# Optimization experiments

Measured on AMD Instinct MI355X. Metric: run time of the kernel, lower is better.

## Reference

```python
import jax, jax.numpy as jnp
import numpy as np

B, S, E, L = 4, 4096, 1024, 64
SCALE = float(np.sqrt(L))


def setup_inputs() -> dict:
    key = jax.random.key(0)
    ks = jax.random.split(key, 7)
    x = jax.random.normal(ks[0], (B, S, E), dtype=jnp.float32)
    # causal mask: positions with mask==0 are disallowed (masked_fill semantics)
    mask = jnp.tril(jnp.ones((S, S), dtype=jnp.int32))
    # Linear params (torch Linear: y = x @ W.T + b); store as [E, L] for x @ W
    sd = 1.0 / np.sqrt(E)
    Wq = jax.random.uniform(ks[1], (E, L), jnp.float32, -sd, sd)
    Wk = jax.random.uniform(ks[2], (E, L), jnp.float32, -sd, sd)
    Wv = jax.random.uniform(ks[3], (E, L), jnp.float32, -sd, sd)
    bq = jax.random.uniform(ks[4], (L,), jnp.float32, -sd, sd)
    bk = jax.random.uniform(ks[5], (L,), jnp.float32, -sd, sd)
    bv = jax.random.uniform(ks[6], (L,), jnp.float32, -sd, sd)
    return {"x": x, "Wq": Wq, "Wk": Wk, "Wv": Wv,
            "bq": bq, "bk": bk, "bv": bv, "mask": mask}


def reference(x, Wq, Wk, Wv, bq, bk, bv, mask):
    # Q,K,V: [B, S, L]
    Q = x @ Wq + bq
    K = x @ Wk + bk
    V = x @ Wv + bv
    # scores: [B, S, S] -- naive full matrix, faithful to the original
    scores = jnp.einsum('bsl,btl->bst', Q, K) / SCALE
    scores = jnp.where(mask == 0, -jnp.inf, scores)
    attn = jax.nn.softmax(scores, axis=-1)
    return jnp.einsum('bst,btl->bsl', attn, V)
```

## Files before the change

kernel.cpp:

```cpp
#include <hip/hip_runtime.h>
#include <hip/hip_bf16.h>
#include <cstdint>

typedef __bf16 bf16_t;
typedef __bf16 bf16x8 __attribute__((ext_vector_type(8)));
typedef float f32x4 __attribute__((ext_vector_type(4)));

#define B_ 4
#define S_ 4096
#define E_ 1024
#define L_ 64

__device__ __forceinline__ f32x4 mfma16(bf16x8 a, bf16x8 b, f32x4 c) {
  return __builtin_amdgcn_mfma_f32_16x16x32_bf16(a, b, c, 0, 0, 0);
}

template <int CTRL>
__device__ __forceinline__ float dpp_max_step(float x) {
  int t = __builtin_amdgcn_update_dpp(0, __float_as_int(x), CTRL, 0xF, 0xF, true);
  return fmaxf(x, __int_as_float(t));
}
template <int CTRL>
__device__ __forceinline__ float dpp_add_step(float x) {
  int t = __builtin_amdgcn_update_dpp(0, __float_as_int(x), CTRL, 0xF, 0xF, true);
  return x + __int_as_float(t);
}
__device__ __forceinline__ float dpp_reduce_max16(float x) {
  x = dpp_max_step<0x121>(x);
  x = dpp_max_step<0x122>(x);
  x = dpp_max_step<0x124>(x);
  x = dpp_max_step<0x128>(x);
  return x;
}
__device__ __forceinline__ float dpp_reduce_add16(float x) {
  x = dpp_add_step<0x121>(x);
  x = dpp_add_step<0x122>(x);
  x = dpp_add_step<0x124>(x);
  x = dpp_add_step<0x128>(x);
  return x;
}


__global__ void prep_w_kernel(const float* __restrict__ Wq, const float* __restrict__ Wk,
                              const float* __restrict__ Wv, bf16_t* __restrict__ Wf) {
  int n = blockIdx.x;
  const float* W = (n < 64) ? Wq : (n < 128 ? Wk : Wv);
  int col = n & 63;
  int nt = n >> 4, lr = n & 15;
  for (int k = threadIdx.x; k < E_; k += blockDim.x) {
    int kt = k >> 5, lg = (k >> 3) & 3, e = k & 7;
    Wf[((size_t)((nt * 32 + kt) * 64 + lg * 16 + lr) << 3) + e] = (bf16_t)W[(size_t)k * L_ + col];
  }
}

__global__ __launch_bounds__(512) void qkv_proj_kernel(
    const float* __restrict__ x, const bf16_t* __restrict__ Wf,
    const float* __restrict__ bq, const float* __restrict__ bk, const float* __restrict__ bv,
    bf16_t* __restrict__ Qf, bf16_t* __restrict__ Kf, bf16_t* __restrict__ Vf) {
  __shared__ float xs[2][32][68];

  const int tid = threadIdx.x;
  const int w = tid >> 6, l = tid & 63;
  const int lr = l & 15, lg = l >> 4;
  const int rowgrp = w & 1, colgrp = w >> 1;
  const int m0b = blockIdx.x * 32;
  const int srow = tid >> 4, scol = (tid & 15) * 4;

  f32x4 acc[3];
#pragma unroll
  for (int t = 0; t < 3; ++t) acc[t] = f32x4{0.f, 0.f, 0.f, 0.f};

  const float* xsrc = x + (size_t)(m0b + srow) * E_ + scol;
  {
    float4 r = *reinterpret_cast<const float4*>(xsrc);
    *reinterpret_cast<float4*>(&xs[0][srow][scol]) = r;
  }
  __syncthreads();

  int buf = 0;
  for (int kc = 0; kc < E_; kc += 64) {
    float4 nx;
    const bool have = (kc + 64) < E_;
    if (have) nx = *reinterpret_cast<const float4*>(xsrc + kc + 64);

    const float* xr = &xs[buf][rowgrp * 16 + lr][0];
    float4 f0 = *reinterpret_cast<const float4*>(xr + lg * 8);
    float4 f1 = *reinterpret_cast<const float4*>(xr + lg * 8 + 4);
    float4 f2 = *reinterpret_cast<const float4*>(xr + 32 + lg * 8);
    float4 f3 = *reinterpret_cast<const float4*>(xr + 32 + lg * 8 + 4);
    bf16x8 a0, a1;
    a0[0] = (bf16_t)f0.x; a0[1] = (bf16_t)f0.y; a0[2] = (bf16_t)f0.z; a0[3] = (bf16_t)f0.w;
    a0[4] = (bf16_t)f1.x; a0[5] = (bf16_t)f1.y; a0[6] = (bf16_t)f1.z; a0[7] = (bf16_t)f1.w;
    a1[0] = (bf16_t)f2.x; a1[1] = (bf16_t)f2.y; a1[2] = (bf16_t)f2.z; a1[3] = (bf16_t)f2.w;
    a1[4] = (bf16_t)f3.x; a1[5] = (bf16_t)f3.y; a1[6] = (bf16_t)f3.z; a1[7] = (bf16_t)f3.w;

    const int kt0 = kc >> 5;
#pragma unroll
    for (int t = 0; t < 3; ++t) {
      const int nt = colgrp * 3 + t;
      bf16x8 b0 = *reinterpret_cast<const bf16x8*>(Wf + (((size_t)(nt * 32 + kt0) * 64 + l) << 3));
      bf16x8 b1 = *reinterpret_cast<const bf16x8*>(Wf + (((size_t)(nt * 32 + kt0 + 1) * 64 + l) << 3));
      acc[t] = mfma16(a0, b0, acc[t]);
      acc[t] = mfma16(a1, b1, acc[t]);
    }
    if (have) *reinterpret_cast<float4*>(&xs[buf ^ 1][srow][scol]) = nx;
    __syncthreads();
    buf ^= 1;
  }

#pragma unroll
  for (int t = 0; t < 3; ++t) {
    int ng = colgrp * 48 + t * 16 + lr;
    int mat = ng >> 6;
    int ncol = ng & 63;
    const float* bias = (mat == 0) ? bq : (mat == 1 ? bk : bv);
    float bb = bias[ncol];
    const int ktq = ncol >> 5, lgw = (ncol >> 3) & 3, ew = ncol & 7;
    const int vt = ncol >> 4, lrw_v = ncol & 15;
#pragma unroll
    for (int r = 0; r < 4; ++r) {
      int mg = m0b + rowgrp * 16 + lg * 4 + r;
      float v = acc[t][r] + bb;
      if (mat < 2) {
        int rt = mg >> 4, lrw = mg & 15;
        size_t idx = (((size_t)((rt * 2 + ktq) * 64 + lgw * 16 + lrw)) << 3) + ew;
        if (mat == 0) Qf[idx] = (bf16_t)v; else Kf[idx] = (bf16_t)v;
      } else {
        int batch = mg >> 12, sl = mg & (S_ - 1);
        int st = sl >> 5, lgv = (sl >> 3) & 3, ev = sl & 7;
        Vf[((size_t)batch << 18) + (((size_t)((st * 4 + vt) * 64 + lgv * 16 + lrw_v)) << 3) + ev] = (bf16_t)v;
      }
    }
  }
}

__global__ __launch_bounds__(256) void attn_kernel(
    const bf16_t* __restrict__ Qf, const bf16_t* __restrict__ Kf,
    const bf16_t* __restrict__ Vf, float* __restrict__ Opart, float* __restrict__ mlpart) {
  __shared__ __align__(16) bf16_t p_lds[4][16 * 72];
  __shared__ bf16_t od_lds[3][16][68];
  __shared__ float ml_lds[3][16][2];

  const int c = threadIdx.x >> 6, l = threadIdx.x & 63;
  const int lr = l & 15, lg = l >> 4;
  const int u = blockIdx.x;
  const int batch = u & 3;
  const int strip = (u >> 2) & 3;
  const int h = (u >> 4) & 1;
  const int qt = 63 - (u >> 5);
  const int qsi = ((u >> 5) << 4) | (u & 15);
  const int qrow = qt * 64 + strip * 16;
  const size_t qbase = (size_t)batch * S_ + qrow;
  bf16_t* pw = p_lds[c];

  const int rtq = batch * 256 + qt * 4 + strip;
  bf16x8 qa0 = *reinterpret_cast<const bf16x8*>(Qf + (((size_t)(rtq * 2) * 64 + l) << 3));
  bf16x8 qa1 = *reinterpret_cast<const bf16x8*>(Qf + (((size_t)(rtq * 2 + 1) * 64 + l) << 3));
  const bf16_t* Vb = Vf + ((size_t)batch << 18);

  f32x4 o[4];
  float m[4], ssum[4];
#pragma unroll
  for (int rr = 0; rr < 4; ++rr) { o[rr] = f32x4{0.f, 0.f, 0.f, 0.f}; m[rr] = -1e30f; ssum[rr] = 0.f; }

  for (int kt = 2 * c + h; kt <= qt; kt += 8) {
    const int t0 = kt * 64;
    f32x4 st[4];
#pragma unroll
    for (int cf = 0; cf < 4; ++cf) st[cf] = f32x4{0.f, 0.f, 0.f, 0.f};
#pragma unroll
    for (int cf = 0; cf < 4; ++cf) {
      const int rtk = batch * 256 + kt * 4 + cf;
      bf16x8 b0 = *reinterpret_cast<const bf16x8*>(Kf + (((size_t)(rtk * 2) * 64 + l) << 3));
      bf16x8 b1 = *reinterpret_cast<const bf16x8*>(Kf + (((size_t)(rtk * 2 + 1) * 64 + l) << 3));
      st[cf] = mfma16(qa0, b0, st[cf]);
      st[cf] = mfma16(qa1, b1, st[cf]);
    }
    const bool diag = (kt == qt);
    float p[4][4];
#pragma unroll
    for (int rr = 0; rr < 4; ++rr) {
      const int qg = qrow + lg * 4 + rr;
      float rowmax = -1e30f;
#pragma unroll
      for (int cf = 0; cf < 4; ++cf) {
        float s = st[cf][rr] * 0.125f;
        if (diag && (t0 + cf * 16 + lr) > qg) s = -1e30f;
        p[cf][rr] = s;
        rowmax = fmaxf(rowmax, s);
      }
      rowmax = dpp_reduce_max16(rowmax);
      float mnew = fmaxf(m[rr], rowmax);
      float scale = __expf(m[rr] - mnew);
      float rs = 0.f;
#pragma unroll
      for (int cf = 0; cf < 4; ++cf) {
        float e = __expf(p[cf][rr] - mnew);
        p[cf][rr] = e;
        rs += e;
      }
      rs = dpp_reduce_add16(rs);
      ssum[rr] = ssum[rr] * scale + rs;
#pragma unroll
      for (int cf = 0; cf < 4; ++cf) o[cf][rr] *= scale;
      m[rr] = mnew;
    }
#pragma unroll
    for (int rr = 0; rr < 4; ++rr)
#pragma unroll
      for (int cf = 0; cf < 4; ++cf)
        pw[(lg * 4 + rr) * 72 + cf * 16 + lr] = (bf16_t)p[cf][rr];
    bf16x8 pa0 = *reinterpret_cast<const bf16x8*>(pw + lr * 72 + lg * 8);
    bf16x8 pa1 = *reinterpret_cast<const bf16x8*>(pw + lr * 72 + 32 + lg * 8);
    const int st0 = kt * 2;
#pragma unroll
    for (int cf = 0; cf < 4; ++cf) {
      bf16x8 v0 = *reinterpret_cast<const bf16x8*>(Vb + (((size_t)((st0 * 4 + cf) * 64 + l)) << 3));
      bf16x8 v1 = *reinterpret_cast<const bf16x8*>(Vb + (((size_t)(((st0 + 1) * 4 + cf) * 64 + l)) << 3));
      o[cf] = mfma16(pa0, v0, o[cf]);
      o[cf] = mfma16(pa1, v1, o[cf]);
    }
  }

  if (c > 0) {
    if (lr == 0) {
#pragma unroll
      for (int rr = 0; rr < 4; ++rr) {
        ml_lds[c - 1][lg * 4 + rr][0] = m[rr];
        ml_lds[c - 1][lg * 4 + rr][1] = ssum[rr];
      }
    }
#pragma unroll
    for (int cf = 0; cf < 4; ++cf)
#pragma unroll
      for (int rr = 0; rr < 4; ++rr)
        od_lds[c - 1][lg * 4 + rr][cf * 16 + lr] = (bf16_t)o[cf][rr];
  }
  __syncthreads();
  if (c == 0) {
    float* Op = Opart + (size_t)(h * 1024 + qsi) * 1024;
    float* mlp = mlpart + (size_t)(h * 1024 + qsi) * 32;
#pragma unroll
    for (int rr = 0; rr < 4; ++rr) {
      const int row = lg * 4 + rr;
      float M = m[rr];
      float mv[3];
#pragma unroll
      for (int cc = 0; cc < 3; ++cc) {
        mv[cc] = ml_lds[cc][row][0];
        M = fmaxf(M, mv[cc]);
      }
      float f0 = __expf(m[rr] - M);
      float Lsum = ssum[rr] * f0;
      float fc[3];
#pragma unroll
      for (int cc = 0; cc < 3; ++cc) {
        fc[cc] = __expf(mv[cc] - M);
        Lsum += ml_lds[cc][row][1] * fc[cc];
      }
      if (lr == 0) { mlp[row * 2] = M; mlp[row * 2 + 1] = Lsum; }
#pragma unroll
      for (int cf = 0; cf < 4; ++cf) {
        float val = o[cf][rr] * f0;
#pragma unroll
        for (int cc = 0; cc < 3; ++cc)
          val += (float)od_lds[cc][row][cf * 16 + lr] * fc[cc];
        Op[row * 64 + cf * 16 + lr] = val;
      }
    }
  }
}

__global__ __launch_bounds__(64) void combine_kernel(
    const float* __restrict__ Opart, const float* __restrict__ mlpart,
    float* __restrict__ out) {
  const int b = blockIdx.x;
  const int batch = b & 3, strip = (b >> 2) & 3, qt = 63 - (b >> 4);
  const int l = threadIdx.x;
  const int row = l >> 2, c0 = (l & 3) * 16;
  const float* ml0 = mlpart + ((size_t)(0 * 1024 + b) * 16 + row) * 2;
  const float* ml1 = mlpart + ((size_t)(1 * 1024 + b) * 16 + row) * 2;
  float m0 = ml0[0], l0 = ml0[1], m1 = ml1[0], l1 = ml1[1];
  float M = fmaxf(m0, m1);
  float f0 = __expf(m0 - M), f1 = __expf(m1 - M);
  float inv = 1.f / (l0 * f0 + l1 * f1);
  const float* O0 = Opart + (size_t)(0 * 1024 + b) * 1024 + row * 64 + c0;
  const float* O1 = Opart + (size_t)(1 * 1024 + b) * 1024 + row * 64 + c0;
  float* dst = out + ((size_t)batch * S_ + qt * 64 + strip * 16 + row) * L_ + c0;
#pragma unroll
  for (int j = 0; j < 4; ++j) {
    float4 a = reinterpret_cast<const float4*>(O0)[j];
    float4 bb = reinterpret_cast<const float4*>(O1)[j];
    float4 v;
    v.x = (a.x * f0 + bb.x * f1) * inv;
    v.y = (a.y * f0 + bb.y * f1) * inv;
    v.z = (a.z * f0 + bb.z * f1) * inv;
    v.w = (a.w * f0 + bb.w * f1) * inv;
    reinterpret_cast<float4*>(dst)[j] = v;
  }
}

extern "C" void kernel_launch(void* const* d_in, const int* in_sizes, int n_in,
                              void* d_out, int out_size, void* d_ws, size_t ws_size,
                              hipStream_t stream) {
  (void)in_sizes; (void)n_in; (void)out_size; (void)ws_size;
  const float* x  = (const float*)d_in[0];
  const float* Wq = (const float*)d_in[1];
  const float* Wk = (const float*)d_in[2];
  const float* Wv = (const float*)d_in[3];
  const float* bq = (const float*)d_in[4];
  const float* bk = (const float*)d_in[5];
  const float* bv = (const float*)d_in[6];
  float* out = (float*)d_out;

  char* ws = (char*)d_ws;
  bf16_t* Qf  = (bf16_t*)(ws + 0);
  bf16_t* Kf  = (bf16_t*)(ws + (size_t)2 * 1024 * 1024);
  bf16_t* Vf  = (bf16_t*)(ws + (size_t)4 * 1024 * 1024);
  bf16_t* Wf  = (bf16_t*)(ws + (size_t)6 * 1024 * 1024);
  float* Opart = (float*)(ws + (size_t)7 * 1024 * 1024);
  float* mlpart = (float*)(ws + (size_t)15 * 1024 * 1024);

  hipLaunchKernelGGL(prep_w_kernel, dim3(192), dim3(256), 0, stream, Wq, Wk, Wv, Wf);
  hipLaunchKernelGGL(qkv_proj_kernel, dim3(16384 / 32), dim3(512), 0, stream,
                     x, Wf, bq, bk, bv, Qf, Kf, Vf);
  hipLaunchKernelGGL(attn_kernel, dim3(2048), dim3(256), 0, stream,
                     Qf, Kf, Vf, Opart, mlpart);
  hipLaunchKernelGGL(combine_kernel, dim3(1024), dim3(64), 0, stream,
                     Opart, mlpart, out);
}
```

Measured before the change: 68.04 us.

## Stage x as bf16 in LDS with wider K chunks and two-deep prefetch

The QKV projection now converts x to bf16 once, when it is staged into shared memory, instead of each wave converting fp32 values after reading them from LDS. The K chunk per iteration grows from 64 to 128, which halves the number of barriers. Global loads are prefetched two iterations ahead and written to the alternate buffer before compute, so load latency overlaps the MFMAs. Holding the prefetched values costs extra registers.

```diff
diff --git a/kernel.cpp b/kernel.cpp
--- a/kernel.cpp
+++ b/kernel.cpp
@@ -57,53 +57,57 @@
     const float* __restrict__ x, const bf16_t* __restrict__ Wf,
     const float* __restrict__ bq, const float* __restrict__ bk, const float* __restrict__ bv,
     bf16_t* __restrict__ Qf, bf16_t* __restrict__ Kf, bf16_t* __restrict__ Vf) {
-  __shared__ float xs[2][32][68];
+  __shared__ __align__(16) bf16_t xs[2][32][136];
 
   const int tid = threadIdx.x;
   const int w = tid >> 6, l = tid & 63;
   const int lr = l & 15, lg = l >> 4;
   const int rowgrp = w & 1, colgrp = w >> 1;
   const int m0b = blockIdx.x * 32;
-  const int srow = tid >> 4, scol = (tid & 15) * 4;
+  const int srow = tid >> 4, scol = (tid & 15) * 8;
 
   f32x4 acc[3];
 #pragma unroll
   for (int t = 0; t < 3; ++t) acc[t] = f32x4{0.f, 0.f, 0.f, 0.f};
 
   const float* xsrc = x + (size_t)(m0b + srow) * E_ + scol;
+
   {
-    float4 r = *reinterpret_cast<const float4*>(xsrc);
-    *reinterpret_cast<float4*>(&xs[0][srow][scol]) = r;
-  }
+    float4 u0 = *reinterpret_cast<const float4*>(xsrc);
+    float4 u1 = *reinterpret_cast<const float4*>(xsrc + 4);
+    bf16x8 pk;
+    pk[0] = (bf16_t)u0.x; pk[1] = (bf16_t)u0.y; pk[2] = (bf16_t)u0.z; pk[3] = (bf16_t)u0.w;
+    pk[4] = (bf16_t)u1.x; pk[5] = (bf16_t)u1.y; pk[6] = (bf16_t)u1.z; pk[7] = (bf16_t)u1.w;
+    *reinterpret_cast<bf16x8*>(&xs[0][srow][scol]) = pk;
+  }
+  float4 v0 = *reinterpret_cast<const float4*>(xsrc + 128);
+  float4 v1 = *reinterpret_cast<const float4*>(xsrc + 132);
   __syncthreads();
 
   int buf = 0;
-  for (int kc = 0; kc < E_; kc += 64) {
-    float4 nx;
-    const bool have = (kc + 64) < E_;
-    if (have) nx = *reinterpret_cast<const float4*>(xsrc + kc + 64);
-
-    const float* xr = &xs[buf][rowgrp * 16 + lr][0];
-    float4 f0 = *reinterpret_cast<const float4*>(xr + lg * 8);
-    float4 f1 = *reinterpret_cast<const float4*>(xr + lg * 8 + 4);
-    float4 f2 = *reinterpret_cast<const float4*>(xr + 32 + lg * 8);
-    float4 f3 = *reinterpret_cast<const float4*>(xr + 32 + lg * 8 + 4);
-    bf16x8 a0, a1;
-    a0[0] = (bf16_t)f0.x; a0[1] = (bf16_t)f0.y; a0[2] = (bf16_t)f0.z; a0[3] = (bf16_t)f0.w;
-    a0[4] = (bf16_t)f1.x; a0[5] = (bf16_t)f1.y; a0[6] = (bf16_t)f1.z; a0[7] = (bf16_t)f1.w;
-    a1[0] = (bf16_t)f2.x; a1[1] = (bf16_t)f2.y; a1[2] = (bf16_t)f2.z; a1[3] = (bf16_t)f2.w;
-    a1[4] = (bf16_t)f3.x; a1[5] = (bf16_t)f3.y; a1[6] = (bf16_t)f3.z; a1[7] = (bf16_t)f3.w;
-
-    const int kt0 = kc >> 5;
-#pragma unroll
-    for (int t = 0; t < 3; ++t) {
-      const int nt = colgrp * 3 + t;
-      bf16x8 b0 = *reinterpret_cast<const bf16x8*>(Wf + (((size_t)(nt * 32 + kt0) * 64 + l) << 3));
-      bf16x8 b1 = *reinterpret_cast<const bf16x8*>(Wf + (((size_t)(nt * 32 + kt0 + 1) * 64 + l) << 3));
-      acc[t] = mfma16(a0, b0, acc[t]);
-      acc[t] = mfma16(a1, b1, acc[t]);
-    }
-    if (have) *reinterpret_cast<float4*>(&xs[buf ^ 1][srow][scol]) = nx;
+  for (int it = 0; it < 8; ++it) {
+    if (it + 1 < 8) {
+      bf16x8 pk;
+      pk[0] = (bf16_t)v0.x; pk[1] = (bf16_t)v0.y; pk[2] = (bf16_t)v0.z; pk[3] = (bf16_t)v0.w;
+      pk[4] = (bf16_t)v1.x; pk[5] = (bf16_t)v1.y; pk[6] = (bf16_t)v1.z; pk[7] = (bf16_t)v1.w;
+      *reinterpret_cast<bf16x8*>(&xs[buf ^ 1][srow][scol]) = pk;
+    }
+    if (it + 2 < 8) {
+      v0 = *reinterpret_cast<const float4*>(xsrc + (it + 2) * 128);
+      v1 = *reinterpret_cast<const float4*>(xsrc + (it + 2) * 128 + 4);
+    }
+    const bf16_t* xr = &xs[buf][rowgrp * 16 + lr][0];
+#pragma unroll
+    for (int ks = 0; ks < 4; ++ks) {
+      bf16x8 a = *reinterpret_cast<const bf16x8*>(xr + ks * 32 + lg * 8);
+      const int kt = it * 4 + ks;
+#pragma unroll
+      for (int t = 0; t < 3; ++t) {
+        const int nt = colgrp * 3 + t;
+        bf16x8 b = *reinterpret_cast<const bf16x8*>(Wf + (((size_t)(nt * 32 + kt) * 64 + l) << 3));
+        acc[t] = mfma16(a, b, acc[t]);
+      }
+    }
     __syncthreads();
     buf ^= 1;
   }
```

Measured after the change: 61.90 us. 9.0% less time.
